# Kernel tuning notes

Hardware: AMD Instinct MI355X
Metric: run time of the kernel (lower is better)

Reference implementation:

```python
import jax, jax.numpy as jnp
import numpy as np

B, C, IC, H, W = 16, 256, 128, 32, 32  # batch, in_channels, inter_channels, spatial
EPS = 1e-5


def _conv1x1(x, w, b=None):
    # x: [B,C,H,W], w: [O,C] -> [B,O,H,W]
    y = jnp.einsum('bchw,oc->bohw', x, w)
    if b is not None:
        y = y + b[None, :, None, None]
    return y


def _dot_kernel(x, wt, wp):
    # relu-matmul attention, symmetrized, degree-rsqrt normalized with zero masking
    b, _, h, w = x.shape
    n = h * w
    t = jnp.maximum(_conv1x1(x, wt), 0.0).reshape(b, -1, n)  # [B,IC,N]
    p = jnp.maximum(_conv1x1(x, wp), 0.0).reshape(b, -1, n)  # [B,IC,N]
    att = jnp.einsum('bcn,bcm->bnm', t, p)                    # [B,N,N]
    att = (att + att.transpose(0, 2, 1)) * 0.5
    d = att.sum(axis=2)                                       # [B,N]
    dinv = jnp.where(d != 0, jax.lax.rsqrt(jnp.where(d != 0, d, 1.0)), 0.0)
    return att * dinv[:, None, :] * dinv[:, :, None]


def _bn(x, gamma, beta):
    # BatchNorm2d in training mode (batch statistics, biased variance)
    mu = jnp.mean(x, axis=(0, 2, 3), keepdims=True)
    var = jnp.mean((x - mu) ** 2, axis=(0, 2, 3), keepdims=True)
    xhat = (x - mu) * jax.lax.rsqrt(var + EPS)
    return xhat * gamma[None, :, None, None] + beta[None, :, None, None]


def setup_inputs() -> dict:
    key = jax.random.key(0)
    ks = jax.random.split(key, 32)
    s = 0.05
    inp = {
        'x':  jax.random.normal(ks[0], (B, C, H, W), jnp.float32),
        'ob': jax.random.normal(ks[1], (B, C, H, W), jnp.float32),
        'od': jax.random.normal(ks[2], (B, C, H, W), jnp.float32),
        'Wt': jax.random.normal(ks[3], (IC, C), jnp.float32) * s,
        'Wp': jax.random.normal(ks[4], (IC, C), jnp.float32) * s,
        'Wgx': jax.random.normal(ks[5], (IC, C), jnp.float32) * s,
        'bgx': jax.random.normal(ks[6], (IC,), jnp.float32) * s,
        'Wgb': jax.random.normal(ks[7], (IC, C), jnp.float32) * s,
        'bgb': jax.random.normal(ks[8], (IC,), jnp.float32) * s,
        'Wgd': jax.random.normal(ks[9], (IC, C), jnp.float32) * s,
        'bgd': jax.random.normal(ks[10], (IC,), jnp.float32) * s,
        'Wwx': jax.random.normal(ks[11], (C, IC), jnp.float32) * s,
        'bwx': jax.random.normal(ks[12], (C,), jnp.float32) * s,
        'Wwb': jax.random.normal(ks[13], (C, IC), jnp.float32) * s,
        'bwb': jax.random.normal(ks[14], (C,), jnp.float32) * s,
        'Wwd': jax.random.normal(ks[15], (C, IC), jnp.float32) * s,
        'bwd': jax.random.normal(ks[16], (C,), jnp.float32) * s,
        'Wwxb': jax.random.normal(ks[17], (C, IC), jnp.float32) * s,
        'bwxb': jax.random.normal(ks[18], (C,), jnp.float32) * s,
        'Wwxd': jax.random.normal(ks[19], (C, IC), jnp.float32) * s,
        'bwxd': jax.random.normal(ks[20], (C,), jnp.float32) * s,
        'gamma1': jnp.ones((C,), jnp.float32),
        'beta1': jnp.zeros((C,), jnp.float32),
        'gamma2': jnp.ones((C,), jnp.float32),
        'beta2': jnp.zeros((C,), jnp.float32),
        'Wout': jax.random.normal(ks[21], (C, C), jnp.float32) * s,
        'bout': jax.random.normal(ks[22], (C,), jnp.float32) * s,
    }
    return inp


def reference(x, ob, od, Wt, Wp, Wgx, bgx, Wgb, bgb, Wgd, bgd,
              Wwx, bwx, Wwb, bwb, Wwd, bwd, Wwxb, bwxb, Wwxd, bwxd,
              gamma1, beta1, gamma2, beta2, Wout, bout):
    b, c, h, w = x.shape
    n = h * w

    def g_tokens(inp, wg, bg):
        return _conv1x1(inp, wg, bg).reshape(b, -1, n).transpose(0, 2, 1)  # [B,N,IC]

    g_x = g_tokens(x, Wgx, bgx)
    g_b = g_tokens(ob, Wgb, bgb)
    g_d = g_tokens(od, Wgd, bgd)

    f_x = _dot_kernel(x, Wt, Wp)
    f_b = _dot_kernel(ob, Wt, Wp)
    f_d = _dot_kernel(od, Wt, Wp)

    def agg(f, g):
        # bmm(f,g).transpose(1,2).view(B,IC,H,W)
        return jnp.einsum('bnm,bmi->bin', f, g).reshape(b, -1, h, w)

    x_self = _conv1x1(agg(f_x, g_x), Wwx, bwx)
    ob_self = _conv1x1(agg(f_b, g_b), Wwb, bwb)
    od_self = _conv1x1(agg(f_d, g_d), Wwd, bwd)
    x_ob_cross = _conv1x1(agg(f_b, g_x), Wwxb, bwxb)
    x_od_cross = _conv1x1(agg(f_d, g_x), Wwxd, bwxd)

    od_final = _bn(od_self + x_ob_cross, gamma1, beta1)
    ob_final = _bn(ob_self + x_od_cross, gamma2, beta2)
    output = _conv1x1(od_final + ob_final + x_self, Wout, bout)
    return output + x
```

## Files before the change

### kernel.cpp

```cpp
#include <hip/hip_runtime.h>

#define GAS __attribute__((address_space(1)))
#define LAS __attribute__((address_space(3)))

typedef __attribute__((ext_vector_type(8))) short short8;
typedef __attribute__((ext_vector_type(4))) float f32x4;
typedef unsigned short u16;

constexpr int cB = 16, cC = 256, cIC = 128, cN = 1024;

__device__ __forceinline__ u16 f2bf(float v) {
    unsigned u = __builtin_bit_cast(unsigned, v);
    return (u16)((u + 0x7fffu + ((u >> 16) & 1u)) >> 16);
}
__device__ __forceinline__ float bf2f(u16 v) {
    unsigned u = ((unsigned)v) << 16;
    return __builtin_bit_cast(float, u);
}
__device__ __forceinline__ float rsz(float d) {
    return (d != 0.0f) ? rsqrtf(d) : 0.0f;
}

template<int N> __device__ __forceinline__ void wait_vmcnt() {
    if constexpr (N == 0) asm volatile("s_waitcnt vmcnt(0)" ::: "memory");
    else if constexpr (N == 1) asm volatile("s_waitcnt vmcnt(1)" ::: "memory");
    else if constexpr (N == 2) asm volatile("s_waitcnt vmcnt(2)" ::: "memory");
    else if constexpr (N == 3) asm volatile("s_waitcnt vmcnt(3)" ::: "memory");
    else if constexpr (N == 4) asm volatile("s_waitcnt vmcnt(4)" ::: "memory");
    else if constexpr (N == 5) asm volatile("s_waitcnt vmcnt(5)" ::: "memory");
    else if constexpr (N == 6) asm volatile("s_waitcnt vmcnt(6)" ::: "memory");
}

template<int BM, int BN, int WR, int WC>
__device__ __forceinline__ void gemm_core(
    const u16* __restrict__ Ab, const u16* __restrict__ Ab2, int ksplit, int lda,
    const u16* __restrict__ Bb, int ldb, int K,
    u16* lsA, u16* lsB,
    f32x4 (&acc)[BM/(WR*16)][BN/(WC*16)])
{
    constexpr int THREADS = WR * WC * 64;
    constexpr int MR = BM / (WR * 16), NR = BN / (WC * 16);
    constexpr int ACH = (BM * 64) / (THREADS * 16);
    constexpr int BCH = (BN * 64) / (THREADS * 16);
    constexpr int RPC = THREADS / 4;
    constexpr int ISSUES = ACH + BCH;

    const int tid  = threadIdx.x;
    const int lane = tid & 63;
    const int wave = tid >> 6;
    const int wr = wave / WC, wc = wave % WC;
    const int r0 = tid >> 2, slot = tid & 3;

    auto stage = [&](int buf, int kk) {
        const u16* Ak = (Ab2 != nullptr && kk >= ksplit) ? (Ab2 + (kk - ksplit)) : (Ab + kk);
        const u16* Bk = Bb + kk;
        #pragma unroll
        for (int c = 0; c < ACH; c++) {
            int row = c * RPC + r0;
            int sk = (slot ^ ((row >> 1) & 3)) << 3;
            __builtin_amdgcn_global_load_lds((GAS void*)(Ak + (size_t)row * lda + sk),
                (LAS void*)(lsA + buf * (BM * 32) + c * (THREADS * 8) + (wave << 9)), 16, 0, 0);
        }
        #pragma unroll
        for (int c = 0; c < BCH; c++) {
            int row = c * RPC + r0;
            int sk = (slot ^ ((row >> 1) & 3)) << 3;
            __builtin_amdgcn_global_load_lds((GAS void*)(Bk + (size_t)row * ldb + sk),
                (LAS void*)(lsB + buf * (BN * 32) + c * (THREADS * 8) + (wave << 9)), 16, 0, 0);
        }
    };

    stage(0, 0);
    const int nt = K >> 5;
    for (int t = 0; t < nt; t++) {
        const int cur = t & 1;
        if (t + 1 < nt) { stage(cur ^ 1, (t + 1) << 5); wait_vmcnt<ISSUES>(); }
        else            wait_vmcnt<0>();
        __builtin_amdgcn_s_barrier();
        asm volatile("" ::: "memory");

        const u16* la = lsA + cur * (BM * 32);
        const u16* lb = lsB + cur * (BN * 32);
        short8 af[MR], bf[NR];
        #pragma unroll
        for (int m = 0; m < MR; m++) {
            int row = wr * (BM / WR) + (m << 4) + (lane & 15);
            af[m] = *(const short8*)&la[(row << 5) + (((lane >> 4) ^ ((row >> 1) & 3)) << 3)];
        }
        #pragma unroll
        for (int n = 0; n < NR; n++) {
            int row = wc * (BN / WC) + (n << 4) + (lane & 15);
            bf[n] = *(const short8*)&lb[(row << 5) + (((lane >> 4) ^ ((row >> 1) & 3)) << 3)];
        }
        #pragma unroll
        for (int m = 0; m < MR; m++)
            #pragma unroll
            for (int n = 0; n < NR; n++)
                acc[m][n] = __builtin_amdgcn_mfma_f32_16x16x32_bf16(af[m], bf[n], acc[m][n], 0, 0, 0);

        asm volatile("s_waitcnt lgkmcnt(0)" ::: "memory");
        __builtin_amdgcn_sched_barrier(0);
        __builtin_amdgcn_s_barrier();
    }
}

template<int BM, int BN, int WR, int WC, bool RELU, bool OBF16, bool RBIAS, bool RESID, bool RSUM>
__global__ __launch_bounds__(WR*WC*64) void gemm_bt(
    const u16* __restrict__ A, long long sA, long long sA2, int lda,
    const u16* __restrict__ B, long long sB, long long sB2, int ldb,
    void* __restrict__ C, long long sC, long long sC2, int ldc,
    int K,
    const float* __restrict__ bias, int sb2,
    const float* __restrict__ resid, long long sR,
    float* __restrict__ rsum, int rsStride)
{
    __shared__ alignas(16) u16 lsA[2 * BM * 32];
    __shared__ alignas(16) u16 lsB[2 * BN * 32];

    const int lane = threadIdx.x & 63;
    const int wave = threadIdx.x >> 6;
    const int wr = wave / WC, wc = wave % WC;
    const int zlo = blockIdx.z & 15, zhi = blockIdx.z >> 4;

    const u16* Ab = A + zlo * sA + zhi * sA2 + (size_t)(blockIdx.x * BM) * lda;
    const u16* Bb = B + zlo * sB + zhi * sB2 + (size_t)(blockIdx.y * BN) * ldb;

    f32x4 acc[BM/(WR*16)][BN/(WC*16)] = {};
    gemm_core<BM, BN, WR, WC>(Ab, nullptr, K, lda, Bb, ldb, K, lsA, lsB, acc);

    const int rowb = blockIdx.x * BM + wr * (BM / WR) + ((lane >> 4) << 2);
    const int colb = blockIdx.y * BN + wc * (BN / WC) + (lane & 15);
    const long long cbase = zlo * sC + zhi * sC2;
    float rp[BM/(WR*16)][4] = {};
    #pragma unroll
    for (int m = 0; m < BM/(WR*16); m++) {
        #pragma unroll
        for (int n = 0; n < BN/(WC*16); n++) {
            #pragma unroll
            for (int r = 0; r < 4; r++) {
                int row = rowb + m * 16 + r;
                int col = colb + n * 16;
                float v = acc[m][n][r];
                if (RBIAS) v += bias[zhi * sb2 + row];
                if (RESID) v += resid[zlo * sR + (size_t)row * ldc + col];
                if (RELU)  v = fmaxf(v, 0.0f);
                if (RSUM)  rp[m][r] += v;
                if (OBF16) ((u16*)C)[cbase + (size_t)row * ldc + col] = f2bf(v);
                else       ((float*)C)[cbase + (size_t)row * ldc + col] = v;
            }
        }
    }
    if (RSUM) {
        #pragma unroll
        for (int m = 0; m < BM/(WR*16); m++) {
            #pragma unroll
            for (int r = 0; r < 4; r++) {
                float v = rp[m][r];
                v += __shfl_xor(v, 1, 64);
                v += __shfl_xor(v, 2, 64);
                v += __shfl_xor(v, 4, 64);
                v += __shfl_xor(v, 8, 64);
                if ((lane & 15) == 0)
                    atomicAdd(&rsum[(size_t)blockIdx.z * rsStride + rowb + m * 16 + r], v);
            }
        }
    }
}

__global__ __launch_bounds__(512) void phase2(
    const u16* __restrict__ XT, const u16* __restrict__ WTP, const u16* __restrict__ WG,
    const float* __restrict__ BG, const float* __restrict__ DINV,
    u16* __restrict__ TPS, u16* __restrict__ GXp, u16* __restrict__ GBp, u16* __restrict__ GDp)
{
    __shared__ alignas(16) u16 lsA[2 * 128 * 32];
    __shared__ alignas(16) u16 lsB[2 * 256 * 32];

    const int id = blockIdx.x;
    const bool tp_path = (id < 384);
    int xb, yb, zs;
    if (tp_path) { xb = id & 7; zs = id >> 3; yb = 0; }
    else         { int g = id - 384; yb = g & 3; zs = g >> 2; xb = 0; }
    const int stream = zs >> 4, b = zs & 15;

    const u16* Ab;
    const u16* Bb;
    if (tp_path) {
        Ab = XT + (size_t)zs * 262144 + (size_t)(xb * 128) * 256;
        Bb = WTP;
    } else {
        Ab = WG + stream * 32768;
        Bb = XT + (size_t)zs * 262144 + (size_t)(yb * 256) * 256;
    }

    f32x4 acc[4][4] = {};
    gemm_core<128, 256, 2, 4>(Ab, nullptr, 256, 256, Bb, 256, 256, lsA, lsB, acc);

    const int lane = threadIdx.x & 63;
    const int wave = threadIdx.x >> 6;
    const int wr = wave >> 2, wc = wave & 3;

    if (tp_path) {
        const int rowb = xb * 128 + wr * 64 + ((lane >> 4) << 2);
        const int colb = wc * 64 + (lane & 15);
        const float* dvr = DINV + stream * 16384 + (b << 10);
        u16* Cb = TPS + (size_t)zs * 262144;
        #pragma unroll
        for (int m = 0; m < 4; m++) {
            #pragma unroll
            for (int r = 0; r < 4; r++) {
                int row = rowb + m * 16 + r;
                float s = rsz(dvr[row]);
                #pragma unroll
                for (int n = 0; n < 4; n++)
                    Cb[(size_t)row * 256 + colb + n * 16] = f2bf(fmaxf(acc[m][n][r], 0.0f) * s);
            }
        }
    } else {
        const int rowb = wr * 64 + ((lane >> 4) << 2);
        const int colb = yb * 256 + wc * 64 + (lane & 15);
        const float* dvx = DINV + (b << 10);
        const float* dvb = DINV + 16384 + (b << 10);
        const float* dvd = DINV + 32768 + (b << 10);
        float sx[4], sb_[4], sd[4];
        #pragma unroll
        for (int n = 0; n < 4; n++) {
            int col = colb + n * 16;
            if (stream == 0) { sx[n] = rsz(dvx[col]); sb_[n] = rsz(dvb[col]); sd[n] = rsz(dvd[col]); }
            else if (stream == 1) sb_[n] = rsz(dvb[col]);
            else sd[n] = rsz(dvd[col]);
        }
        #pragma unroll
        for (int m = 0; m < 4; m++) {
            #pragma unroll
            for (int r = 0; r < 4; r++) {
                int row = rowb + m * 16 + r;
                float bias = BG[stream * 128 + row];
                #pragma unroll
                for (int n = 0; n < 4; n++) {
                    int col = colb + n * 16;
                    float v = acc[m][n][r] + bias;
                    if (stream == 0) {
                        GXp[(size_t)b * 131072 + ((size_t)row << 10) + col] = f2bf(v * sx[n]);
                        GBp[(size_t)b * 262144 + ((size_t)(row + 128) << 10) + col] = f2bf(v * sb_[n]);
                        GDp[(size_t)b * 262144 + ((size_t)(row + 128) << 10) + col] = f2bf(v * sd[n]);
                    } else if (stream == 1) {
                        GBp[(size_t)b * 262144 + ((size_t)row << 10) + col] = f2bf(v * sb_[n]);
                    } else {
                        GDp[(size_t)b * 262144 + ((size_t)row << 10) + col] = f2bf(v * sd[n]);
                    }
                }
            }
        }
    }
}

__global__ __launch_bounds__(256) void inner_gemm(
    const u16* __restrict__ TPt, const u16* __restrict__ GXp,
    const u16* __restrict__ GBp, const u16* __restrict__ GDp,
    u16* __restrict__ MX, u16* __restrict__ MB, u16* __restrict__ MD)
{
    __shared__ alignas(16) u16 lsA[2 * 128 * 32];
    __shared__ alignas(16) u16 lsB[2 * 128 * 32];

    const int z = blockIdx.z, which = z >> 4, b = z & 15;
    if (which == 0 && blockIdx.y != 0) return;
    const u16* Gp = (which == 0) ? GXp : (which == 1) ? GBp : GDp;
    u16* M = (which == 0) ? MX : (which == 1) ? MB : MD;
    const int ldc = (which == 0) ? 128 : 256;
    const long long sB = (which == 0) ? 131072 : 262144;

    const u16* Ab = TPt + (size_t)z * 262144 + (size_t)(blockIdx.x * 128) * 1024;
    const u16* Bb = Gp + (size_t)b * sB + (size_t)(blockIdx.y * 128) * 1024;

    f32x4 acc[4][4] = {};
    gemm_core<128, 128, 2, 2>(Ab, nullptr, 1024, 1024, Bb, 1024, 1024, lsA, lsB, acc);

    const int lane = threadIdx.x & 63;
    const int wave = threadIdx.x >> 6;
    const int wr = wave >> 1, wc = wave & 1;
    const int rowb = blockIdx.x * 128 + (wr << 6) + ((lane >> 4) << 2);
    const int colb = blockIdx.y * 128 + (wc << 6) + (lane & 15);
    u16* Cb = M + (size_t)b * (256 * ldc);
    #pragma unroll
    for (int m = 0; m < 4; m++)
        #pragma unroll
        for (int n = 0; n < 4; n++)
            #pragma unroll
            for (int r = 0; r < 4; r++) {
                int row = (rowb + m * 16 + r) ^ 128;
                int col = colb + n * 16;
                Cb[(size_t)row * ldc + col] = f2bf(acc[m][n][r]);
            }
}

__global__ __launch_bounds__(512) void fold_gemm(
    const u16* __restrict__ WF, const u16* __restrict__ MX,
    const u16* __restrict__ MB, const u16* __restrict__ MD,
    u16* __restrict__ FF2)
{
    __shared__ alignas(16) u16 lsA[2 * 128 * 32];
    __shared__ alignas(16) u16 lsB[2 * 256 * 32];

    const int z = blockIdx.z, q = z >> 4, b = z & 15;
    const int pair = (q >> 1) + (q == 4 ? 0 : 0) * 0 + ((q == 4) ? 2 : (q >> 1));
    const int pr = (q == 4) ? 2 : (q >> 1);
    const int side = (q == 1 || q == 3) ? 1 : 0;
    (void)pair;
    const u16* Mp = (q == 4) ? MX : (q == 1 || q == 2) ? MB : MD;
    const int coff = (q == 1 || q == 3) ? 128 : 0;
    const int ldb  = (q == 4) ? 128 : 256;

    const u16* Ab = WF + q * 32768 + (size_t)(blockIdx.x * 128) * 128;
    const u16* Bb = Mp + (size_t)b * (256 * ldb) + coff;

    f32x4 acc[4][4] = {};
    gemm_core<128, 256, 2, 4>(Ab, nullptr, 128, 128, Bb, ldb, 128, lsA, lsB, acc);

    const int lane = threadIdx.x & 63;
    const int wave = threadIdx.x >> 6;
    const int wr = wave >> 2, wc = wave & 3;
    const int rowb = blockIdx.x * 128 + wr * 64 + ((lane >> 4) << 2);
    const int colb = side * 256 + wc * 64 + (lane & 15);
    u16* Cb = FF2 + (size_t)pr * 2097152 + (size_t)b * 131072;
    #pragma unroll
    for (int m = 0; m < 4; m++)
        #pragma unroll
        for (int n = 0; n < 4; n++)
            #pragma unroll
            for (int r = 0; r < 4; r++)
                Cb[(size_t)(rowb + m * 16 + r) * 512 + colb + n * 16] = f2bf(acc[m][n][r]);
}

__global__ __launch_bounds__(512) void outer_gemm(
    const u16* __restrict__ TPS, const u16* __restrict__ FF2,
    u16* __restrict__ S1b, u16* __restrict__ S2b, u16* __restrict__ XSb)
{
    __shared__ alignas(16) u16 lsA[2 * 128 * 32];
    __shared__ alignas(16) u16 lsB[2 * 256 * 32];

    const int z = blockIdx.z, zhi = z >> 4, b = z & 15;
    const int sa1[3] = {2, 1, 0}, sa2[3] = {1, 2, 0};
    const int K = (zhi == 2) ? 256 : 512;

    const u16* A1 = TPS + (size_t)(sa1[zhi] * 16 + b) * 262144 + (size_t)(blockIdx.x * 128) * 256;
    const u16* A2 = (zhi == 2) ? nullptr
                  : TPS + (size_t)(sa2[zhi] * 16 + b) * 262144 + (size_t)(blockIdx.x * 128) * 256;
    const u16* Bb = FF2 + (size_t)zhi * 2097152 + (size_t)b * 131072;

    f32x4 acc[4][4] = {};
    gemm_core<128, 256, 2, 4>(A1, A2, 256, 256, Bb, 512, K, lsA, lsB, acc);

    const int lane = threadIdx.x & 63;
    const int wave = threadIdx.x >> 6;
    const int wr = wave >> 2, wc = wave & 3;
    const int rowb = blockIdx.x * 128 + wr * 64 + ((lane >> 4) << 2);
    const int colb = wc * 64 + (lane & 15);
    u16* Cb = ((zhi == 0) ? S1b : (zhi == 1) ? S2b : XSb) + (size_t)b * 262144;
    #pragma unroll
    for (int m = 0; m < 4; m++)
        #pragma unroll
        for (int n = 0; n < 4; n++)
            #pragma unroll
            for (int r = 0; r < 4; r++)
                Cb[(size_t)(rowb + m * 16 + r) * 256 + colb + n * 16] = f2bf(acc[m][n][r]);
}

__global__ void prep_transpose(const float* __restrict__ x, const float* __restrict__ ob,
                               const float* __restrict__ od, u16* __restrict__ xt,
                               const float* Wt, const float* Wp,
                               const float* Wgx, const float* Wgb, const float* Wgd,
                               const float* bgx, const float* bgb, const float* bgd,
                               const float* Wwd, const float* Wwxb, const float* Wwb,
                               const float* Wwxd, const float* Wwx, const float* Wout,
                               u16* wtp, u16* wg, u16* wf, u16* wout, float* bg,
                               float* __restrict__ ZZ)
{
    int tx = threadIdx.x, ty = threadIdx.y;
    if (blockIdx.z == 48) {
        int t = (blockIdx.y * 32 + blockIdx.x) * 256 + ty * 32 + tx;
        wtp[t]  = f2bf(t < 32768 ? Wt[t] : Wp[t - 32768]);
        wout[t] = f2bf(Wout[t]);
        if (t < 32768) {
            wg[t] = f2bf(Wgx[t]); wg[32768 + t] = f2bf(Wgb[t]); wg[65536 + t] = f2bf(Wgd[t]);
            wf[t]          = f2bf(0.5f * Wwd[t]);
            wf[32768 + t]  = f2bf(0.5f * Wwxb[t]);
            wf[65536 + t]  = f2bf(0.5f * Wwb[t]);
            wf[98304 + t]  = f2bf(0.5f * Wwxd[t]);
            wf[131072 + t] = f2bf(0.5f * Wwx[t]);
        }
        if (t < 384) bg[t] = (t < 128) ? bgx[t] : (t < 256) ? bgb[t - 128] : bgd[t - 256];
        if (t < 62464) ZZ[t] = 0.0f;
        return;
    }
    __shared__ float tbuf[32][33];
    int z = blockIdx.z, which = z >> 4, b = z & 15;
    const float* src = (which == 0) ? x : (which == 1) ? ob : od;
    const float* s = src + (size_t)b * cC * cN;
    u16* dst = xt + (size_t)which * (cB * cN * cC) + (size_t)b * (cN * cC);
    int n0 = blockIdx.x << 5, c0 = blockIdx.y << 5;
    #pragma unroll
    for (int i = 0; i < 4; i++) { int r = ty + (i << 3); tbuf[r][tx] = s[(size_t)(c0 + r) * cN + n0 + tx]; }
    __syncthreads();
    #pragma unroll
    for (int i = 0; i < 4; i++) { int r = ty + (i << 3); dst[(size_t)(n0 + r) * cC + c0 + tx] = f2bf(tbuf[tx][r]); }
}

__global__ void dinv_partial(const u16* __restrict__ TPt, const float* __restrict__ CS,
                             float* __restrict__ DINV)
{
    int z = blockIdx.y;
    int cq = blockIdx.z;
    int n = blockIdx.x * 256 + threadIdx.x;
    __shared__ float ws[64];
    if (threadIdx.x < 64) {
        int c = cq * 64 + threadIdx.x;
        ws[threadIdx.x] = 0.5f * CS[z * 256 + (c ^ 128)];
    }
    __syncthreads();
    const u16* base = TPt + (size_t)z * 262144 + (size_t)(cq * 64) * 1024 + n;
    float d = 0;
    #pragma unroll 16
    for (int c = 0; c < 64; c++) d += bf2f(base[(size_t)c << 10]) * ws[c];
    atomicAdd(&DINV[(z << 10) + n], d);
}

__global__ void bn_stats(const u16* __restrict__ s1, const u16* __restrict__ s2,
                         float* __restrict__ acc)
{
    int c = threadIdx.x;
    const u16* s = blockIdx.y ? s2 : s1;
    float* a = acc + blockIdx.y * 512;
    size_t r0 = (size_t)blockIdx.x * 64;
    float sum = 0, sq = 0;
    for (int r = 0; r < 64; r++) { float v = bf2f(s[(r0 + r) * 256 + c]); sum += v; sq += v * v; }
    atomicAdd(&a[c], sum);
    atomicAdd(&a[256 + c], sq);
}

__global__ void combine_kernel(const u16* __restrict__ s1, const u16* __restrict__ s2,
                               const u16* __restrict__ xs, const float* __restrict__ BNA,
                               const float* __restrict__ g1, const float* __restrict__ be1,
                               const float* __restrict__ g2, const float* __restrict__ be2,
                               const float* __restrict__ bwx, u16* __restrict__ pre)
{
    size_t t = (size_t)blockIdx.x * 256 + threadIdx.x;
    size_t base = t << 3;
    int c0 = (int)(base & 255);
    short8 a = *(const short8*)(s1 + base);
    short8 b = *(const short8*)(s2 + base);
    short8 cx = *(const short8*)(xs + base);
    const float inv = 1.0f / 16384.0f;
    short8 o;
    #pragma unroll
    for (int j = 0; j < 8; j++) {
        int c = c0 + j;
        float m1 = BNA[c] * inv;
        float v1 = BNA[256 + c] * inv - m1 * m1;
        float sc1 = g1[c] * rsqrtf(v1 + 1e-5f);
        float sh1 = be1[c] - m1 * sc1;
        float m2 = BNA[512 + c] * inv;
        float v2 = BNA[768 + c] * inv - m2 * m2;
        float sc2 = g2[c] * rsqrtf(v2 + 1e-5f);
        float sh2 = be2[c] - m2 * sc2;
        float v = sc1 * bf2f((u16)a[j]) + sh1 + sc2 * bf2f((u16)b[j]) + sh2
                + bf2f((u16)cx[j]) + bwx[c];
        o[j] = (short)f2bf(v);
    }
    *(short8*)(pre + base) = o;
}

extern "C" void kernel_launch(void* const* d_in, const int* in_sizes, int n_in,
                              void* d_out, int out_size, void* d_ws, size_t ws_size,
                              hipStream_t stream)
{
    const float* x    = (const float*)d_in[0];
    const float* ob   = (const float*)d_in[1];
    const float* od   = (const float*)d_in[2];
    const float* Wt   = (const float*)d_in[3];
    const float* Wp   = (const float*)d_in[4];
    const float* Wgx  = (const float*)d_in[5];
    const float* bgx  = (const float*)d_in[6];
    const float* Wgb  = (const float*)d_in[7];
    const float* bgb  = (const float*)d_in[8];
    const float* Wgd  = (const float*)d_in[9];
    const float* bgd  = (const float*)d_in[10];
    const float* Wwx  = (const float*)d_in[11];
    const float* bwx  = (const float*)d_in[12];
    const float* Wwb  = (const float*)d_in[13];
    const float* Wwd  = (const float*)d_in[15];
    const float* Wwxb = (const float*)d_in[17];
    const float* Wwxd = (const float*)d_in[19];
    const float* g1   = (const float*)d_in[21];
    const float* be1  = (const float*)d_in[22];
    const float* g2   = (const float*)d_in[23];
    const float* be2  = (const float*)d_in[24];
    const float* Wout = (const float*)d_in[25];
    const float* bout = (const float*)d_in[26];
    float* out = (float*)d_out;

    char* w = (char*)d_ws;
    u16*   XT   = (u16*)(w);
    u16*   TPt  = (u16*)(w + 25165824);
    u16*   TPS  = (u16*)(w + 50331648);
    u16*   GXp  = (u16*)(w + 75497472);
    u16*   GBp  = (u16*)(w + 79691776);
    u16*   GDp  = (u16*)(w + 88080384);
    u16*   MX   = (u16*)(w + 96468992);
    u16*   MB   = (u16*)(w + 97517568);
    u16*   MD   = (u16*)(w + 99614720);
    u16*   FF2  = (u16*)(w + 101711872);
    u16*   S1b  = (u16*)(w + 114294784);
    u16*   S2b  = (u16*)(w + 122683392);
    u16*   XSb  = (u16*)(w + 131072000);
    u16*   WTP  = (u16*)(w + 139460608);
    u16*   WG   = (u16*)(w + 139591680);
    u16*   WF   = (u16*)(w + 139788288);
    u16*   WOUT = (u16*)(w + 140115968);
    float* BGf  = (float*)(w + 140247040);
    float* ZZ   = (float*)(w + 140249088);

    float* CS   = ZZ;
    float* DINV = ZZ + 12288;
    float* BNA  = ZZ + 61440;
    u16*   PRE  = TPt;

    prep_transpose<<<dim3(32, 8, 49), dim3(32, 8), 0, stream>>>(
        x, ob, od, XT, Wt, Wp, Wgx, Wgb, Wgd, bgx, bgb, bgd,
        Wwd, Wwxb, Wwb, Wwxd, Wwx, Wout, WTP, WG, WF, WOUT, BGf, ZZ);

    gemm_bt<128, 256, 2, 4, true, true, false, false, true><<<dim3(2, 4, 48), 512, 0, stream>>>(
        WTP, 0, 0, 256,  XT, 262144, 4194304, 256,  TPt, 262144, 4194304, 1024,
        256, nullptr, 0, nullptr, 0, CS, 256);

    dinv_partial<<<dim3(4, 48, 4), 256, 0, stream>>>(TPt, CS, DINV);

    phase2<<<dim3(576), 512, 0, stream>>>(XT, WTP, WG, BGf, DINV, TPS, GXp, GBp, GDp);

    inner_gemm<<<dim3(2, 2, 48), 256, 0, stream>>>(TPt, GXp, GBp, GDp, MX, MB, MD);

    fold_gemm<<<dim3(2, 1, 80), 512, 0, stream>>>(WF, MX, MB, MD, FF2);

    outer_gemm<<<dim3(8, 1, 48), 512, 0, stream>>>(TPS, FF2, S1b, S2b, XSb);

    bn_stats<<<dim3(256, 2), 256, 0, stream>>>(S1b, S2b, BNA);

    combine_kernel<<<dim3(2048), 256, 0, stream>>>(S1b, S2b, XSb, BNA,
        g1, be1, g2, be2, bwx, PRE);

    gemm_bt<128, 256, 2, 4, false, false, true, true, false><<<dim3(2, 4, 16), 512, 0, stream>>>(
        WOUT, 0, 0, 256,  PRE, 262144, 0, 256,  out, 262144, 0, 1024,
        256, bout, 0, x, 262144, nullptr, 0);
}
```

Measured before the change: 166.9 us.

## Fuse degree, BatchNorm stats and combine into GEMM epilogues and final GEMM

Computes the degree normalisation inside a new phase2a GEMM epilogue (reduced in shared memory) instead of a separate dinv_partial pass, and splits phase2 into two launches so G-token scaling can read the fresh DINV. outer_gemm now writes the S1/S2/XS results interleaved into one K=768 buffer and accumulates BatchNorm sums and squares via atomics. A small bnscale kernel folds the BN scale into the output weights and the shifts into a bias, so the final GEMM runs with K=768 and the bn_stats and combine kernels are removed. This saves several full-tensor read/write passes, at the cost of a larger final GEMM and one extra launch.

```diff
diff --git a/kernel.cpp b/kernel.cpp
--- a/kernel.cpp
+++ b/kernel.cpp
@@ -167,87 +167,136 @@
     }
 }
 
-__global__ __launch_bounds__(512) void phase2(
-    const u16* __restrict__ XT, const u16* __restrict__ WTP, const u16* __restrict__ WG,
-    const float* __restrict__ BG, const float* __restrict__ DINV,
-    u16* __restrict__ TPS, u16* __restrict__ GXp, u16* __restrict__ GBp, u16* __restrict__ GDp)
+__global__ __launch_bounds__(512) void phase2a(
+    const u16* __restrict__ XT, const u16* __restrict__ WTP,
+    const float* __restrict__ CS,
+    u16* __restrict__ TPS, float* __restrict__ DINV)
 {
     __shared__ alignas(16) u16 lsA[2 * 128 * 32];
     __shared__ alignas(16) u16 lsB[2 * 256 * 32];
-
-    const int id = blockIdx.x;
-    const bool tp_path = (id < 384);
-    int xb, yb, zs;
-    if (tp_path) { xb = id & 7; zs = id >> 3; yb = 0; }
-    else         { int g = id - 384; yb = g & 3; zs = g >> 2; xb = 0; }
-    const int stream = zs >> 4, b = zs & 15;
-
-    const u16* Ab;
-    const u16* Bb;
-    if (tp_path) {
-        Ab = XT + (size_t)zs * 262144 + (size_t)(xb * 128) * 256;
-        Bb = WTP;
-    } else {
-        Ab = WG + stream * 32768;
-        Bb = XT + (size_t)zs * 262144 + (size_t)(yb * 256) * 256;
-    }
+    __shared__ float part[128][4];
+
+    const int xb = blockIdx.x, zs = blockIdx.z;
+    const u16* Ab = XT + (size_t)zs * 262144 + (size_t)(xb * 128) * 256;
 
     f32x4 acc[4][4] = {};
-    gemm_core<128, 256, 2, 4>(Ab, nullptr, 256, 256, Bb, 256, 256, lsA, lsB, acc);
+    gemm_core<128, 256, 2, 4>(Ab, nullptr, 256, 256, WTP, 256, 256, lsA, lsB, acc);
 
     const int lane = threadIdx.x & 63;
     const int wave = threadIdx.x >> 6;
     const int wr = wave >> 2, wc = wave & 3;
-
-    if (tp_path) {
-        const int rowb = xb * 128 + wr * 64 + ((lane >> 4) << 2);
-        const int colb = wc * 64 + (lane & 15);
-        const float* dvr = DINV + stream * 16384 + (b << 10);
-        u16* Cb = TPS + (size_t)zs * 262144;
-        #pragma unroll
-        for (int m = 0; m < 4; m++) {
-            #pragma unroll
-            for (int r = 0; r < 4; r++) {
-                int row = rowb + m * 16 + r;
-                float s = rsz(dvr[row]);
-                #pragma unroll
-                for (int n = 0; n < 4; n++)
-                    Cb[(size_t)row * 256 + colb + n * 16] = f2bf(fmaxf(acc[m][n][r], 0.0f) * s);
-            }
-        }
-    } else {
-        const int rowb = wr * 64 + ((lane >> 4) << 2);
-        const int colb = yb * 256 + wc * 64 + (lane & 15);
-        const float* dvx = DINV + (b << 10);
-        const float* dvb = DINV + 16384 + (b << 10);
-        const float* dvd = DINV + 32768 + (b << 10);
-        float sx[4], sb_[4], sd[4];
-        #pragma unroll
-        for (int n = 0; n < 4; n++) {
-            int col = colb + n * 16;
-            if (stream == 0) { sx[n] = rsz(dvx[col]); sb_[n] = rsz(dvb[col]); sd[n] = rsz(dvd[col]); }
-            else if (stream == 1) sb_[n] = rsz(dvb[col]);
-            else sd[n] = rsz(dvd[col]);
-        }
-        #pragma unroll
-        for (int m = 0; m < 4; m++) {
-            #pragma unroll
-            for (int r = 0; r < 4; r++) {
-                int row = rowb + m * 16 + r;
-                float bias = BG[stream * 128 + row];
-                #pragma unroll
-                for (int n = 0; n < 4; n++) {
-                    int col = colb + n * 16;
-                    float v = acc[m][n][r] + bias;
-                    if (stream == 0) {
-                        GXp[(size_t)b * 131072 + ((size_t)row << 10) + col] = f2bf(v * sx[n]);
-                        GBp[(size_t)b * 262144 + ((size_t)(row + 128) << 10) + col] = f2bf(v * sb_[n]);
-                        GDp[(size_t)b * 262144 + ((size_t)(row + 128) << 10) + col] = f2bf(v * sd[n]);
-                    } else if (stream == 1) {
-                        GBp[(size_t)b * 262144 + ((size_t)row << 10) + col] = f2bf(v * sb_[n]);
-                    } else {
-                        GDp[(size_t)b * 262144 + ((size_t)row << 10) + col] = f2bf(v * sd[n]);
-                    }
+    const int lrow0 = wr * 64 + ((lane >> 4) << 2);
+    const int colb = wc * 64 + (lane & 15);
+
+    float wsv[4];
+    #pragma unroll
+    for (int n = 0; n < 4; n++) wsv[n] = 0.5f * CS[zs * 256 + ((colb + n * 16) ^ 128)];
+
+    float pd[4][4];
+    #pragma unroll
+    for (int m = 0; m < 4; m++) {
+        #pragma unroll
+        for (int r = 0; r < 4; r++) {
+            float s = 0;
+            #pragma unroll
+            for (int n = 0; n < 4; n++) {
+                float v = fmaxf(acc[m][n][r], 0.0f);
+                acc[m][n][r] = v;
+                s += v * wsv[n];
+            }
+            pd[m][r] = s;
+        }
+    }
+    #pragma unroll
+    for (int m = 0; m < 4; m++) {
+        #pragma unroll
+        for (int r = 0; r < 4; r++) {
+            float v = pd[m][r];
+            v += __shfl_xor(v, 1, 64);
+            v += __shfl_xor(v, 2, 64);
+            v += __shfl_xor(v, 4, 64);
+            v += __shfl_xor(v, 8, 64);
+            pd[m][r] = v;
+        }
+    }
+    if ((lane & 15) == 0) {
+        #pragma unroll
+        for (int m = 0; m < 4; m++)
+            #pragma unroll
+            for (int r = 0; r < 4; r++)
+                part[lrow0 + m * 16 + r][wc] = pd[m][r];
+    }
+    __syncthreads();
+
+    u16* Cb = TPS + (size_t)zs * 262144;
+    float* dout = DINV + (zs << 10) + xb * 128;
+    #pragma unroll
+    for (int m = 0; m < 4; m++) {
+        #pragma unroll
+        for (int r = 0; r < 4; r++) {
+            int lrow = lrow0 + m * 16 + r;
+            float d = part[lrow][0] + part[lrow][1] + part[lrow][2] + part[lrow][3];
+            if (wc == 0 && (lane & 15) == 0) dout[lrow] = d;
+            float dv = rsz(d);
+            size_t rbase = (size_t)(xb * 128 + lrow) * 256;
+            #pragma unroll
+            for (int n = 0; n < 4; n++)
+                Cb[rbase + colb + n * 16] = f2bf(acc[m][n][r] * dv);
+        }
+    }
+}
+
+__global__ __launch_bounds__(512) void phase2b(
+    const u16* __restrict__ XT, const u16* __restrict__ WG,
+    const float* __restrict__ BG, const float* __restrict__ DINV,
+    u16* __restrict__ GXp, u16* __restrict__ GBp, u16* __restrict__ GDp)
+{
+    __shared__ alignas(16) u16 lsA[2 * 128 * 32];
+    __shared__ alignas(16) u16 lsB[2 * 256 * 32];
+
+    const int yb = blockIdx.x, zs = blockIdx.z;
+    const int stream = zs >> 4, b = zs & 15;
+
+    const u16* Ab = WG + stream * 32768;
+    const u16* Bb = XT + (size_t)zs * 262144 + (size_t)(yb * 256) * 256;
+
+    f32x4 acc[4][4] = {};
+    gemm_core<128, 256, 2, 4>(Ab, nullptr, 256, 256, Bb, 256, 256, lsA, lsB, acc);
+
+    const int lane = threadIdx.x & 63;
+    const int wave = threadIdx.x >> 6;
+    const int wr = wave >> 2, wc = wave & 3;
+    const int rowb = wr * 64 + ((lane >> 4) << 2);
+    const int colb = yb * 256 + wc * 64 + (lane & 15);
+    const float* dvx = DINV + (b << 10);
+    const float* dvb = DINV + 16384 + (b << 10);
+    const float* dvd = DINV + 32768 + (b << 10);
+    float sx[4], sb_[4], sd[4];
+    #pragma unroll
+    for (int n = 0; n < 4; n++) {
+        int col = colb + n * 16;
+        if (stream == 0) { sx[n] = rsz(dvx[col]); sb_[n] = rsz(dvb[col]); sd[n] = rsz(dvd[col]); }
+        else if (stream == 1) sb_[n] = rsz(dvb[col]);
+        else sd[n] = rsz(dvd[col]);
+    }
+    #pragma unroll
+    for (int m = 0; m < 4; m++) {
+        #pragma unroll
+        for (int r = 0; r < 4; r++) {
+            int row = rowb + m * 16 + r;
+            float bias = BG[stream * 128 + row];
+            #pragma unroll
+            for (int n = 0; n < 4; n++) {
+                int col = colb + n * 16;
+                float v = acc[m][n][r] + bias;
+                if (stream == 0) {
+                    GXp[(size_t)b * 131072 + ((size_t)row << 10) + col] = f2bf(v * sx[n]);
+                    GBp[(size_t)b * 262144 + ((size_t)(row + 128) << 10) + col] = f2bf(v * sb_[n]);
+                    GDp[(size_t)b * 262144 + ((size_t)(row + 128) << 10) + col] = f2bf(v * sd[n]);
+                } else if (stream == 1) {
+                    GBp[(size_t)b * 262144 + ((size_t)row << 10) + col] = f2bf(v * sb_[n]);
+                } else {
+                    GDp[(size_t)b * 262144 + ((size_t)row << 10) + col] = f2bf(v * sd[n]);
                 }
             }
         }
@@ -302,10 +351,8 @@
     __shared__ alignas(16) u16 lsB[2 * 256 * 32];
 
     const int z = blockIdx.z, q = z >> 4, b = z & 15;
-    const int pair = (q >> 1) + (q == 4 ? 0 : 0) * 0 + ((q == 4) ? 2 : (q >> 1));
     const int pr = (q == 4) ? 2 : (q >> 1);
     const int side = (q == 1 || q == 3) ? 1 : 0;
-    (void)pair;
     const u16* Mp = (q == 4) ? MX : (q == 1 || q == 2) ? MB : MD;
     const int coff = (q == 1 || q == 3) ? 128 : 0;
     const int ldb  = (q == 4) ? 128 : 256;
@@ -333,7 +380,7 @@
 
 __global__ __launch_bounds__(512) void outer_gemm(
     const u16* __restrict__ TPS, const u16* __restrict__ FF2,
-    u16* __restrict__ S1b, u16* __restrict__ S2b, u16* __restrict__ XSb)
+    u16* __restrict__ SALL, float* __restrict__ BNA)
 {
     __shared__ alignas(16) u16 lsA[2 * 128 * 32];
     __shared__ alignas(16) u16 lsB[2 * 256 * 32];
@@ -355,14 +402,57 @@
     const int wr = wave >> 2, wc = wave & 3;
     const int rowb = blockIdx.x * 128 + wr * 64 + ((lane >> 4) << 2);
     const int colb = wc * 64 + (lane & 15);
-    u16* Cb = ((zhi == 0) ? S1b : (zhi == 1) ? S2b : XSb) + (size_t)b * 262144;
+    u16* Cb = SALL + (size_t)b * 786432;
+
+    float csum[4] = {}, csq[4] = {};
     #pragma unroll
     for (int m = 0; m < 4; m++)
         #pragma unroll
         for (int n = 0; n < 4; n++)
             #pragma unroll
-            for (int r = 0; r < 4; r++)
-                Cb[(size_t)(rowb + m * 16 + r) * 256 + colb + n * 16] = f2bf(acc[m][n][r]);
+            for (int r = 0; r < 4; r++) {
+                float v = acc[m][n][r];
+                Cb[(size_t)(rowb + m * 16 + r) * 768 + zhi * 256 + colb + n * 16] = f2bf(v);
+                csum[n] += v;
+                csq[n] += v * v;
+            }
+    if (zhi < 2) {
+        #pragma unroll
+        for (int n = 0; n < 4; n++) {
+            float s = csum[n], q = csq[n];
+            s += __shfl_xor(s, 16, 64); s += __shfl_xor(s, 32, 64);
+            q += __shfl_xor(q, 16, 64); q += __shfl_xor(q, 32, 64);
+            if (lane < 16) {
+                atomicAdd(&BNA[zhi * 512 + colb + n * 16], s);
+                atomicAdd(&BNA[zhi * 512 + 256 + colb + n * 16], q);
+            }
+        }
+    }
+}
+
+__global__ __launch_bounds__(256) void bnscale(
+    const float* __restrict__ Wout, const float* __restrict__ g1, const float* __restrict__ be1,
+    const float* __restrict__ g2, const float* __restrict__ be2,
+    const float* __restrict__ bwx, const float* __restrict__ bout,
+    const float* __restrict__ BNA, u16* __restrict__ WoutS, float* __restrict__ BIAS2)
+{
+    int o = blockIdx.x, c = threadIdx.x;
+    const float inv = 1.0f / 16384.0f;
+    float m1 = BNA[c] * inv;
+    float v1 = BNA[256 + c] * inv - m1 * m1;
+    float sc1 = g1[c] * rsqrtf(v1 + 1e-5f), sh1 = be1[c] - m1 * sc1;
+    float m2 = BNA[512 + c] * inv;
+    float v2 = BNA[768 + c] * inv - m2 * m2;
+    float sc2 = g2[c] * rsqrtf(v2 + 1e-5f), sh2 = be2[c] - m2 * sc2;
+    float wv = Wout[o * 256 + c];
+    WoutS[o * 768 + c]       = f2bf(wv * sc1);
+    WoutS[o * 768 + 256 + c] = f2bf(wv * sc2);
+    WoutS[o * 768 + 512 + c] = f2bf(wv);
+    __shared__ float red[256];
+    red[c] = wv * (sh1 + sh2 + bwx[c]);
+    __syncthreads();
+    for (int s = 128; s; s >>= 1) { if (c < s) red[c] += red[c + s]; __syncthreads(); }
+    if (c == 0) BIAS2[o] = red[0] + bout[o];
 }
 
 __global__ void prep_transpose(const float* __restrict__ x, const float* __restrict__ ob,
@@ -371,15 +461,14 @@
                                const float* Wgx, const float* Wgb, const float* Wgd,
                                const float* bgx, const float* bgb, const float* bgd,
                                const float* Wwd, const float* Wwxb, const float* Wwb,
-                               const float* Wwxd, const float* Wwx, const float* Wout,
-                               u16* wtp, u16* wg, u16* wf, u16* wout, float* bg,
+                               const float* Wwxd, const float* Wwx,
+                               u16* wtp, u16* wg, u16* wf, float* bg,
                                float* __restrict__ ZZ)
 {
     int tx = threadIdx.x, ty = threadIdx.y;
     if (blockIdx.z == 48) {
         int t = (blockIdx.y * 32 + blockIdx.x) * 256 + ty * 32 + tx;
-        wtp[t]  = f2bf(t < 32768 ? Wt[t] : Wp[t - 32768]);
-        wout[t] = f2bf(Wout[t]);
+        wtp[t] = f2bf(t < 32768 ? Wt[t] : Wp[t - 32768]);
         if (t < 32768) {
             wg[t] = f2bf(Wgx[t]); wg[32768 + t] = f2bf(Wgb[t]); wg[65536 + t] = f2bf(Wgd[t]);
             wf[t]          = f2bf(0.5f * Wwd[t]);
@@ -389,7 +478,7 @@
             wf[131072 + t] = f2bf(0.5f * Wwx[t]);
         }
         if (t < 384) bg[t] = (t < 128) ? bgx[t] : (t < 256) ? bgb[t - 128] : bgd[t - 256];
-        if (t < 62464) ZZ[t] = 0.0f;
+        if (t < 13312) ZZ[t] = 0.0f;
         return;
     }
     __shared__ float tbuf[32][33];
@@ -403,70 +492,6 @@
     __syncthreads();
     #pragma unroll
     for (int i = 0; i < 4; i++) { int r = ty + (i << 3); dst[(size_t)(n0 + r) * cC + c0 + tx] = f2bf(tbuf[tx][r]); }
-}
-
-__global__ void dinv_partial(const u16* __restrict__ TPt, const float* __restrict__ CS,
-                             float* __restrict__ DINV)
-{
-    int z = blockIdx.y;
-    int cq = blockIdx.z;
-    int n = blockIdx.x * 256 + threadIdx.x;
-    __shared__ float ws[64];
-    if (threadIdx.x < 64) {
-        int c = cq * 64 + threadIdx.x;
-        ws[threadIdx.x] = 0.5f * CS[z * 256 + (c ^ 128)];
-    }
-    __syncthreads();
-    const u16* base = TPt + (size_t)z * 262144 + (size_t)(cq * 64) * 1024 + n;
-    float d = 0;
-    #pragma unroll 16
-    for (int c = 0; c < 64; c++) d += bf2f(base[(size_t)c << 10]) * ws[c];
-    atomicAdd(&DINV[(z << 10) + n], d);
-}
-
-__global__ void bn_stats(const u16* __restrict__ s1, const u16* __restrict__ s2,
-                         float* __restrict__ acc)
-{
-    int c = threadIdx.x;
-    const u16* s = blockIdx.y ? s2 : s1;
-    float* a = acc + blockIdx.y * 512;
-    size_t r0 = (size_t)blockIdx.x * 64;
-    float sum = 0, sq = 0;
-    for (int r = 0; r < 64; r++) { float v = bf2f(s[(r0 + r) * 256 + c]); sum += v; sq += v * v; }
-    atomicAdd(&a[c], sum);
-    atomicAdd(&a[256 + c], sq);
-}
-
-__global__ void combine_kernel(const u16* __restrict__ s1, const u16* __restrict__ s2,
-                               const u16* __restrict__ xs, const float* __restrict__ BNA,
-                               const float* __restrict__ g1, const float* __restrict__ be1,
-                               const float* __restrict__ g2, const float* __restrict__ be2,
-                               const float* __restrict__ bwx, u16* __restrict__ pre)
-{
-    size_t t = (size_t)blockIdx.x * 256 + threadIdx.x;
-    size_t base = t << 3;
-    int c0 = (int)(base & 255);
-    short8 a = *(const short8*)(s1 + base);
-    short8 b = *(const short8*)(s2 + base);
-    short8 cx = *(const short8*)(xs + base);
-    const float inv = 1.0f / 16384.0f;
-    short8 o;
-    #pragma unroll
-    for (int j = 0; j < 8; j++) {
-        int c = c0 + j;
-        float m1 = BNA[c] * inv;
-        float v1 = BNA[256 + c] * inv - m1 * m1;
-        float sc1 = g1[c] * rsqrtf(v1 + 1e-5f);
-        float sh1 = be1[c] - m1 * sc1;
-        float m2 = BNA[512 + c] * inv;
-        float v2 = BNA[768 + c] * inv - m2 * m2;
-        float sc2 = g2[c] * rsqrtf(v2 + 1e-5f);
-        float sh2 = be2[c] - m2 * sc2;
-        float v = sc1 * bf2f((u16)a[j]) + sh1 + sc2 * bf2f((u16)b[j]) + sh2
-                + bf2f((u16)cx[j]) + bwx[c];
-        o[j] = (short)f2bf(v);
-    }
-    *(short8*)(pre + base) = o;
 }
 
 extern "C" void kernel_launch(void* const* d_in, const int* in_sizes, int n_in,
@@ -499,55 +524,51 @@
     float* out = (float*)d_out;
 
     char* w = (char*)d_ws;
-    u16*   XT   = (u16*)(w);
-    u16*   TPt  = (u16*)(w + 25165824);
-    u16*   TPS  = (u16*)(w + 50331648);
-    u16*   GXp  = (u16*)(w + 75497472);
-    u16*   GBp  = (u16*)(w + 79691776);
-    u16*   GDp  = (u16*)(w + 88080384);
-    u16*   MX   = (u16*)(w + 96468992);
-    u16*   MB   = (u16*)(w + 97517568);
-    u16*   MD   = (u16*)(w + 99614720);
-    u16*   FF2  = (u16*)(w + 101711872);
-    u16*   S1b  = (u16*)(w + 114294784);
-    u16*   S2b  = (u16*)(w + 122683392);
-    u16*   XSb  = (u16*)(w + 131072000);
-    u16*   WTP  = (u16*)(w + 139460608);
-    u16*   WG   = (u16*)(w + 139591680);
-    u16*   WF   = (u16*)(w + 139788288);
-    u16*   WOUT = (u16*)(w + 140115968);
-    float* BGf  = (float*)(w + 140247040);
-    float* ZZ   = (float*)(w + 140249088);
-
-    float* CS   = ZZ;
-    float* DINV = ZZ + 12288;
-    float* BNA  = ZZ + 61440;
-    u16*   PRE  = TPt;
+    u16*   XT    = (u16*)(w);
+    u16*   TPt   = (u16*)(w + 25165824);
+    u16*   TPS   = (u16*)(w + 50331648);
+    u16*   GXp   = (u16*)(w + 75497472);
+    u16*   GBp   = (u16*)(w + 79691776);
+    u16*   GDp   = (u16*)(w + 88080384);
+    u16*   MX    = (u16*)(w + 96468992);
+    u16*   MB    = (u16*)(w + 97517568);
+    u16*   MD    = (u16*)(w + 99614720);
+    u16*   FF2   = (u16*)(w + 101711872);
+    u16*   WTP   = (u16*)(w + 114294784);
+    u16*   WG    = (u16*)(w + 114425856);
+    u16*   WF    = (u16*)(w + 114622464);
+    u16*   WoutS = (u16*)(w + 114950144);
+    float* BGf   = (float*)(w + 115343360);
+    float* BIAS2 = (float*)(w + 115345408);
+    float* DINV  = (float*)(w + 115349504);
+    float* ZZ    = (float*)(w + 115546112);
+
+    float* CS  = ZZ;
+    float* BNA = ZZ + 12288;
+    u16*   SALL = TPt;
 
     prep_transpose<<<dim3(32, 8, 49), dim3(32, 8), 0, stream>>>(
         x, ob, od, XT, Wt, Wp, Wgx, Wgb, Wgd, bgx, bgb, bgd,
-        Wwd, Wwxb, Wwb, Wwxd, Wwx, Wout, WTP, WG, WF, WOUT, BGf, ZZ);
+        Wwd, Wwxb, Wwb, Wwxd, Wwx, WTP, WG, WF, BGf, ZZ);
 
     gemm_bt<128, 256, 2, 4, true, true, false, false, true><<<dim3(2, 4, 48), 512, 0, stream>>>(
         WTP, 0, 0, 256,  XT, 262144, 4194304, 256,  TPt, 262144, 4194304, 1024,
         256, nullptr, 0, nullptr, 0, CS, 256);
 
-    dinv_partial<<<dim3(4, 48, 4), 256, 0, stream>>>(TPt, CS, DINV);
-
-    phase2<<<dim3(576), 512, 0, stream>>>(XT, WTP, WG, BGf, DINV, TPS, GXp, GBp, GDp);
+    phase2a<<<dim3(8, 1, 48), 512, 0, stream>>>(XT, WTP, CS, TPS, DINV);
+
+    phase2b<<<dim3(4, 1, 48), 512, 0, stream>>>(XT, WG, BGf, DINV, GXp, GBp, GDp);
 
     inner_gemm<<<dim3(2, 2, 48), 256, 0, stream>>>(TPt, GXp, GBp, GDp, MX, MB, MD);
 
     fold_gemm<<<dim3(2, 1, 80), 512, 0, stream>>>(WF, MX, MB, MD, FF2);
 
-    outer_gemm<<<dim3(8, 1, 48), 512, 0, stream>>>(TPS, FF2, S1b, S2b, XSb);
-
-    bn_stats<<<dim3(256, 2), 256, 0, stream>>>(S1b, S2b, BNA);
-
-    combine_kernel<<<dim3(2048), 256, 0, stream>>>(S1b, S2b, XSb, BNA,
-        g1, be1, g2, be2, bwx, PRE);
+    outer_gemm<<<dim3(8, 1, 48), 512, 0, stream>>>(TPS, FF2, SALL, BNA);
+
+    bnscale<<<dim3(256), 256, 0, stream>>>(Wout, g1, be1, g2, be2, bwx, bout,
+                                           BNA, WoutS, BIAS2);
 
     gemm_bt<128, 256, 2, 4, false, false, true, true, false><<<dim3(2, 4, 16), 512, 0, stream>>>(
-        WOUT, 0, 0, 256,  PRE, 262144, 0, 256,  out, 262144, 0, 1024,
-        256, bout, 0, x, 262144, nullptr, 0);
-}
+        WoutS, 0, 0, 768,  SALL, 786432, 0, 768,  out, 262144, 0, 1024,
+        768, BIAS2, 0, x, 262144, nullptr, 0);
+}
```

New measurement: 168.2 us. No clear change (+0.8%).
